# Kernel optimization log

Hardware: AMD Instinct MI355X
Metric: run time of the kernel (lower is better)

## Reference

```python
import jax, jax.numpy as jnp
import numpy as np

N = 50000   # nodes
E = 800000  # edges (avg degree 16)
D = 2048    # resnet50 feature dim
C = 256     # layer_size
NEG_SLOPE = 0.2


def setup_inputs() -> dict:
    key = jax.random.key(0)
    ks = jax.random.split(key, 16)
    s = 0.02
    inp = {
        'x': jax.random.normal(ks[0], (N, D), jnp.float32),
        'edge_index': jax.random.randint(ks[1], (2, E), 0, N, dtype=jnp.int32),
        # GATConv layer 1 (in=D, out=C, heads=1)
        'W1': jax.random.normal(ks[2], (D, C), jnp.float32) * s,
        'a_src1': jax.random.normal(ks[3], (C,), jnp.float32) * s,
        'a_dst1': jax.random.normal(ks[4], (C,), jnp.float32) * s,
        'b1': jnp.zeros((C,), jnp.float32),
        # GATConv layer 2 (in=C, out=C)
        'W2': jax.random.normal(ks[5], (C, C), jnp.float32) * s,
        'a_src2': jax.random.normal(ks[6], (C,), jnp.float32) * s,
        'a_dst2': jax.random.normal(ks[7], (C,), jnp.float32) * s,
        'b2': jnp.zeros((C,), jnp.float32),
        # EdgePredictor: lin1 (2C -> C), lin2 (C -> 1)
        'Wp1': jax.random.normal(ks[8], (2 * C, C), jnp.float32) * s,
        'bp1': jnp.zeros((C,), jnp.float32),
        'wp2': jax.random.normal(ks[9], (C,), jnp.float32) * s,
        'bp2': jnp.zeros((), jnp.float32),
    }
    return inp


def gat_layer(x, src, dst, W, a_src, a_dst, b, n_nodes):
    # PyG GATConv, heads=1, concat=True: message flows src -> dst,
    # softmax over incoming edges of each dst node.
    h = x @ W                                   # [N, C]
    e = jax.nn.leaky_relu((h @ a_src)[src] + (h @ a_dst)[dst], NEG_SLOPE)  # [E]
    emax = jax.ops.segment_max(e, dst, num_segments=n_nodes)
    ex = jnp.exp(e - emax[dst])
    denom = jax.ops.segment_sum(ex, dst, num_segments=n_nodes)
    alpha = ex / (denom[dst] + 1e-16)           # [E]
    out = jax.ops.segment_sum(h[src] * alpha[:, None], dst, num_segments=n_nodes)
    return out + b


def reference(x, edge_index, W1, a_src1, a_dst1, b1, W2, a_src2, a_dst2, b2,
              Wp1, bp1, wp2, bp2):
    src, dst = edge_index[0], edge_index[1]
    # GATConv default add_self_loops=True
    loops = jnp.arange(N, dtype=src.dtype)
    src_sl = jnp.concatenate([src, loops])
    dst_sl = jnp.concatenate([dst, loops])

    h = gat_layer(x, src_sl, dst_sl, W1, a_src1, a_dst1, b1, N)
    h = gat_layer(h, src_sl, dst_sl, W2, a_src2, a_dst2, b2, N)

    # edge predictor on the ORIGINAL edge_index (no self loops)
    xe = jnp.concatenate([h[src], h[dst]], axis=-1)       # [E, 2C]
    z = jax.nn.relu(xe @ Wp1 + bp1)                        # [E, C]  (dropout: eval mode)
    return z @ wp2 + bp2                                   # [E]
```

## Files before the change

kernel.cpp:

```cpp
#include <hip/hip_runtime.h>
#include <hip/hip_bf16.h>
#include <stdint.h>

#define NNODES 50000
#define NEDGES 800000
#define DIN    2048
#define CDIM   256
#define ELOOP  (NEDGES + NNODES)

using bf16x8 = __attribute__((ext_vector_type(8))) short;
using f32x4  = __attribute__((ext_vector_type(4))) float;
using gvoid  = __attribute__((address_space(1))) const void;
using lvoid  = __attribute__((address_space(3))) void;

__device__ __forceinline__ float bf2f(uint16_t u) {
    union { uint32_t i; float f; } v; v.i = (uint32_t)u << 16; return v.f;
}
__device__ __forceinline__ uint16_t f2bf(float f) {
    union { float f; uint32_t i; } v; v.f = f;
    uint32_t i = v.i;
    return (uint16_t)((i + 0x7FFFu + ((i >> 16) & 1u)) >> 16);
}
__device__ __forceinline__ void unpack8(uint4 r, float* f) {
    f[0] = bf2f((uint16_t)(r.x & 0xffffu)); f[1] = bf2f((uint16_t)(r.x >> 16));
    f[2] = bf2f((uint16_t)(r.y & 0xffffu)); f[3] = bf2f((uint16_t)(r.y >> 16));
    f[4] = bf2f((uint16_t)(r.z & 0xffffu)); f[5] = bf2f((uint16_t)(r.z >> 16));
    f[6] = bf2f((uint16_t)(r.w & 0xffffu)); f[7] = bf2f((uint16_t)(r.w >> 16));
}

#define BM 128
#define BN 128
#define BK 32

#define WAITVM(N) asm volatile("s_waitcnt vmcnt(" #N ")" ::: "memory")

#define ROWDOT_EPILOGUE()                                                     \
    if (s_src) {                                                              \
        float av[4], dv[4];                                                   \
        for (int nt2 = 0; nt2 < 4; ++nt2) {                                   \
            int gn = bn + wn + nt2 * 16 + lm;                                 \
            av[nt2] = asrc[gn];                                               \
            dv[nt2] = adst[gn];                                               \
        }                                                                     \
        for (int mt = 0; mt < 4; ++mt)                                        \
            for (int r = 0; r < 4; ++r) {                                     \
                float ps = 0.f, pd = 0.f;                                     \
                for (int nt2 = 0; nt2 < 4; ++nt2) {                           \
                    float v = acc[mt][nt2][r];                                \
                    ps += v * av[nt2];                                        \
                    pd += v * dv[nt2];                                        \
                }                                                             \
                for (int d = 1; d < 16; d <<= 1) {                            \
                    ps += __shfl_xor(ps, d);                                  \
                    pd += __shfl_xor(pd, d);                                  \
                }                                                             \
                if (lm == 0) {                                                \
                    int gm = bm + wm + mt * 16 + lq * 4 + r;                  \
                    if (gm < M) {                                             \
                        atomicAdd(&s_src[gm], ps);                            \
                        atomicAdd(&s_dst[gm], pd);                            \
                    }                                                         \
                }                                                             \
            }                                                                 \
    }

__global__ __launch_bounds__(256)
void gemm_bt(const uint16_t* __restrict__ A, const uint16_t* __restrict__ Bt,
             uint16_t* __restrict__ C, const float* __restrict__ bias,
             const float* __restrict__ asrc, const float* __restrict__ adst,
             float* __restrict__ s_src, float* __restrict__ s_dst,
             int M, int N, int K)
{
    __shared__ __align__(16) uint16_t lA[3][BM * BK];
    __shared__ __align__(16) uint16_t lB[3][BN * BK];
    const int tid  = threadIdx.x;
    const int wave = tid >> 6;
    const int lane = tid & 63;
    const int lm = lane & 15, lq = lane >> 4;
    const int bm = blockIdx.x * BM;
    const int bn = blockIdx.y * BN;
    const int wm = (wave >> 1) * 64;
    const int wn = (wave & 1) * 64;

    f32x4 acc[4][4];
    for (int i = 0; i < 4; ++i)
        for (int j = 0; j < 4; ++j)
            acc[i][j] = (f32x4)0.0f;

    auto stage = [&](int buf, int k0) {
        for (int j = 0; j < 2; ++j) {
            int c = j * 256 + wave * 64 + lane;
            int row = c >> 2, cc = c & 3;
            int gr = bm + row; if (gr >= M) gr = M - 1;
            const uint16_t* gp = A + (size_t)gr * K + k0 + cc * 8;
            __builtin_amdgcn_global_load_lds((gvoid*)gp,
                (lvoid*)(lA[buf] + (size_t)(j * 256 + wave * 64) * 8), 16, 0, 0);
        }
        for (int j = 0; j < 2; ++j) {
            int c = j * 256 + wave * 64 + lane;
            int row = c >> 2, cc = c & 3;
            const uint16_t* gp = Bt + (size_t)(bn + row) * K + k0 + cc * 8;
            __builtin_amdgcn_global_load_lds((gvoid*)gp,
                (lvoid*)(lB[buf] + (size_t)(j * 256 + wave * 64) * 8), 16, 0, 0);
        }
    };

    const int ntiles = K / BK;
    stage(0, 0);
    stage(1, BK);
    WAITVM(4);
    __builtin_amdgcn_s_barrier();

    for (int t = 0; t < ntiles; ++t) {
        const int cur = t % 3;
        if (t + 2 < ntiles) stage((t + 2) % 3, (t + 2) * BK);

        bf16x8 af[4], bfr[4];
        for (int mt = 0; mt < 4; ++mt)
            af[mt] = *(const bf16x8*)(lA[cur] + (wm + mt * 16 + lm) * BK + lq * 8);
        for (int nt2 = 0; nt2 < 4; ++nt2)
            bfr[nt2] = *(const bf16x8*)(lB[cur] + (wn + nt2 * 16 + lm) * BK + lq * 8);

        for (int mt = 0; mt < 4; ++mt)
            for (int nt2 = 0; nt2 < 4; ++nt2)
                acc[mt][nt2] = __builtin_amdgcn_mfma_f32_16x16x32_bf16(
                    af[mt], bfr[nt2], acc[mt][nt2], 0, 0, 0);

        if (t + 1 < ntiles) {
            if (t + 2 < ntiles) WAITVM(4);
            else                WAITVM(0);
            __builtin_amdgcn_s_barrier();
        }
    }

    for (int mt = 0; mt < 4; ++mt) {
        for (int nt2 = 0; nt2 < 4; ++nt2) {
            int gn = bn + wn + nt2 * 16 + lm;
            float badd = bias ? bias[gn] : 0.0f;
            for (int r = 0; r < 4; ++r) {
                int gm = bm + wm + mt * 16 + lq * 4 + r;
                if (gm < M)
                    C[(size_t)gm * N + gn] = f2bf(acc[mt][nt2][r] + badd);
            }
        }
    }

    ROWDOT_EPILOGUE();
}

__global__ __launch_bounds__(256)
void gemm_f32_bt(const float* __restrict__ A, const uint16_t* __restrict__ Bt,
                 uint16_t* __restrict__ C,
                 const float* __restrict__ asrc, const float* __restrict__ adst,
                 float* __restrict__ s_src, float* __restrict__ s_dst,
                 int M, int N, int K)
{
    __shared__ __align__(16) float    lA[3][BM * BK];
    __shared__ __align__(16) uint16_t lB[3][BN * BK];
    const int tid  = threadIdx.x;
    const int wave = tid >> 6;
    const int lane = tid & 63;
    const int lm = lane & 15, lq = lane >> 4;
    const int bm = blockIdx.x * BM;
    const int bn = blockIdx.y * BN;
    const int wm = (wave >> 1) * 64;
    const int wn = (wave & 1) * 64;

    f32x4 acc[4][4];
    for (int i = 0; i < 4; ++i)
        for (int j = 0; j < 4; ++j)
            acc[i][j] = (f32x4)0.0f;

    auto stage = [&](int buf, int k0) {
        for (int j = 0; j < 4; ++j) {
            int c = j * 256 + wave * 64 + lane;
            int row = c >> 3;
            int lc  = (c & 7) ^ (row & 7);
            int gr = bm + row; if (gr >= M) gr = M - 1;
            const float* gp = A + (size_t)gr * K + k0 + lc * 4;
            __builtin_amdgcn_global_load_lds((gvoid*)gp,
                (lvoid*)(lA[buf] + (size_t)(j * 256 + wave * 64) * 4), 16, 0, 0);
        }
        for (int j = 0; j < 2; ++j) {
            int c = j * 256 + wave * 64 + lane;
            int row = c >> 2, cc = c & 3;
            const uint16_t* gp = Bt + (size_t)(bn + row) * K + k0 + cc * 8;
            __builtin_amdgcn_global_load_lds((gvoid*)gp,
                (lvoid*)(lB[buf] + (size_t)(j * 256 + wave * 64) * 8), 16, 0, 0);
        }
    };

    const int ntiles = K / BK;
    stage(0, 0);
    stage(1, BK);
    WAITVM(6);
    __builtin_amdgcn_s_barrier();

    for (int t = 0; t < ntiles; ++t) {
        const int cur = t % 3;
        if (t + 2 < ntiles) stage((t + 2) % 3, (t + 2) * BK);

        bf16x8 af[4], bfr[4];
        for (int mt = 0; mt < 4; ++mt) {
            int r = wm + mt * 16 + lm;
            int s0 = (lq * 2)     ^ (r & 7);
            int s1 = (lq * 2 + 1) ^ (r & 7);
            f32x4 a0 = *(const f32x4*)(lA[cur] + r * BK + s0 * 4);
            f32x4 a1 = *(const f32x4*)(lA[cur] + r * BK + s1 * 4);
            union { uint32_t u[4]; bf16x8 v; } t2;
            float x0 = a0[0], x1 = a0[1], x2 = a0[2], x3 = a0[3];
            float y0 = a1[0], y1 = a1[1], y2 = a1[2], y3 = a1[3];
            asm("v_cvt_pk_bf16_f32 %0, %1, %2" : "=v"(t2.u[0]) : "v"(x0), "v"(x1));
            asm("v_cvt_pk_bf16_f32 %0, %1, %2" : "=v"(t2.u[1]) : "v"(x2), "v"(x3));
            asm("v_cvt_pk_bf16_f32 %0, %1, %2" : "=v"(t2.u[2]) : "v"(y0), "v"(y1));
            asm("v_cvt_pk_bf16_f32 %0, %1, %2" : "=v"(t2.u[3]) : "v"(y2), "v"(y3));
            af[mt] = t2.v;
        }
        for (int nt2 = 0; nt2 < 4; ++nt2)
            bfr[nt2] = *(const bf16x8*)(lB[cur] + (wn + nt2 * 16 + lm) * BK + lq * 8);

        for (int mt = 0; mt < 4; ++mt)
            for (int nt2 = 0; nt2 < 4; ++nt2)
                acc[mt][nt2] = __builtin_amdgcn_mfma_f32_16x16x32_bf16(
                    af[mt], bfr[nt2], acc[mt][nt2], 0, 0, 0);

        if (t + 1 < ntiles) {
            if (t + 2 < ntiles) WAITVM(6);
            else                WAITVM(0);
            __builtin_amdgcn_s_barrier();
        }
    }

    for (int mt = 0; mt < 4; ++mt) {
        for (int nt2 = 0; nt2 < 4; ++nt2) {
            int gn = bn + wn + nt2 * 16 + lm;
            for (int r = 0; r < 4; ++r) {
                int gm = bm + wm + mt * 16 + lq * 4 + r;
                if (gm < M)
                    C[(size_t)gm * N + gn] = f2bf(acc[mt][nt2][r]);
            }
        }
    }

    ROWDOT_EPILOGUE();
}

__global__ __launch_bounds__(256)
void transpose_cvt_kernel(const float* __restrict__ W,
                          uint16_t* __restrict__ Wt, int K, int N)
{
    __shared__ float tile[32][33];
    const int k0 = blockIdx.x * 32, n0 = blockIdx.y * 32;
    const int tx = threadIdx.x & 31, ty = threadIdx.x >> 5;
    for (int r = 0; r < 32; r += 8)
        tile[ty + r][tx] = W[(size_t)(k0 + ty + r) * N + n0 + tx];
    __syncthreads();
    for (int r = 0; r < 32; r += 8)
        Wt[(size_t)(n0 + ty + r) * K + k0 + tx] = f2bf(tile[tx][ty + r]);
}

__global__ void bias512_kernel(const float* __restrict__ bp1,
                               float* __restrict__ bias512)
{
    int i = blockIdx.x * 256 + threadIdx.x;
    if (i < 512) bias512[i] = (i < 256) ? bp1[i] : 0.0f;
}

__global__ void count_kernel(const int* __restrict__ ei, int* __restrict__ rs)
{
    int i = blockIdx.x * 256 + threadIdx.x;
    if (i >= ELOOP) return;
    int dst = (i < NEDGES) ? ei[NEDGES + i] : (i - NEDGES);
    atomicAdd(&rs[dst + 1], 1);
}

__global__ __launch_bounds__(1024)
void scan_part_kernel(int* __restrict__ rs, int* __restrict__ bsum)
{
    __shared__ int wsum[16];
    const int b = blockIdx.x, tid = threadIdx.x, lane = tid & 63, w = tid >> 6;
    int i = b * 1024 + tid;
    int v = (i <= NNODES) ? rs[i] : 0;
    int s = v;
    for (int d = 1; d < 64; d <<= 1) {
        int t = __shfl_up(s, d);
        if (lane >= d) s += t;
    }
    if (lane == 63) wsum[w] = s;
    __syncthreads();
    if (tid < 16) {
        int x = wsum[tid];
        for (int d = 1; d < 16; d <<= 1) {
            int t = __shfl_up(x, d);
            if (tid >= d) x += t;
        }
        wsum[tid] = x;
    }
    __syncthreads();
    int incl = s + (w > 0 ? wsum[w - 1] : 0);
    if (i <= NNODES) rs[i] = incl;
    if (tid == 1023) bsum[b] = incl;
}

__global__ void scan_bsum_kernel(int* __restrict__ bsum, int nb)
{
    int tid = threadIdx.x;
    int v = (tid < nb) ? bsum[tid] : 0;
    for (int d = 1; d < 64; d <<= 1) {
        int t = __shfl_up(v, d);
        if (tid >= d) v += t;
    }
    if (tid < nb) bsum[tid] = v;
}

__global__ __launch_bounds__(1024)
void scan_add_kernel(const int* __restrict__ bsum, int* __restrict__ rs,
                     int* __restrict__ cursor)
{
    int b = blockIdx.x;
    int i = b * 1024 + threadIdx.x;
    int add = b ? bsum[b - 1] : 0;
    if (i <= NNODES) {
        int r = rs[i] + add;
        rs[i] = r;
        if (i < NNODES) cursor[i] = r;
    }
}

__global__ void fill_kernel(const int* __restrict__ ei, int* __restrict__ cursor,
                            int* __restrict__ csr_src, int* __restrict__ csr_eid)
{
    int i = blockIdx.x * 256 + threadIdx.x;
    if (i >= ELOOP) return;
    int src, dst, eid;
    if (i < NEDGES) { src = ei[i]; dst = ei[NEDGES + i]; eid = i; }
    else            { src = dst = i - NEDGES; eid = -1; }
    int pos = atomicAdd(&cursor[dst], 1);
    csr_src[pos] = src;
    csr_eid[pos] = eid;
}

__global__ __launch_bounds__(256)
void attn_kernel(const int* __restrict__ row_start, const int* __restrict__ csr_src,
                 const float* __restrict__ s_src, const float* __restrict__ s_dst,
                 const uint16_t* __restrict__ g, const float* __restrict__ bvec,
                 uint16_t* __restrict__ hout)
{
    int n = blockIdx.x * 4 + (threadIdx.x >> 6);
    int lane = threadIdx.x & 63;
    int beg = row_start[n], end = row_start[n + 1];
    float sdn = s_dst[n];

    float m = -1e30f;
    for (int i = beg + lane; i < end; i += 64) {
        float e = s_src[csr_src[i]] + sdn;
        e = (e > 0.f) ? e : 0.2f * e;
        m = fmaxf(m, e);
    }
    for (int d = 32; d; d >>= 1) m = fmaxf(m, __shfl_xor(m, d));

    float sum = 0.f;
    for (int i = beg + lane; i < end; i += 64) {
        float e = s_src[csr_src[i]] + sdn;
        e = (e > 0.f) ? e : 0.2f * e;
        sum += __expf(e - m);
    }
    for (int d = 32; d; d >>= 1) sum += __shfl_xor(sum, d);
    float inv = 1.f / (sum + 1e-16f);

    const int q = lane >> 4, ql = lane & 15;
    float a[16];
    #pragma unroll
    for (int j = 0; j < 16; ++j) a[j] = 0.f;

    for (int i = beg + q; i < end; i += 4) {
        int src = csr_src[i];
        float e = s_src[src] + sdn;
        e = (e > 0.f) ? e : 0.2f * e;
        float alpha = __expf(e - m) * inv;
        const uint16_t* gp = g + (size_t)src * CDIM + ql * 16;
        uint4 r0 = *(const uint4*)gp;
        uint4 r1 = *(const uint4*)(gp + 8);
        float f0[8], f1[8];
        unpack8(r0, f0); unpack8(r1, f1);
        #pragma unroll
        for (int j = 0; j < 8; ++j) {
            a[j]     += alpha * f0[j];
            a[8 + j] += alpha * f1[j];
        }
    }
    #pragma unroll
    for (int j = 0; j < 16; ++j) {
        a[j] += __shfl_xor(a[j], 16);
        a[j] += __shfl_xor(a[j], 32);
    }

    if (q == 0) {
        const float4 b0 = *(const float4*)(bvec + ql * 16);
        const float4 b1 = *(const float4*)(bvec + ql * 16 + 4);
        const float4 b2 = *(const float4*)(bvec + ql * 16 + 8);
        const float4 b3 = *(const float4*)(bvec + ql * 16 + 12);
        uint4 o0, o1;
        o0.x = (uint32_t)f2bf(a[0]  + b0.x) | ((uint32_t)f2bf(a[1]  + b0.y) << 16);
        o0.y = (uint32_t)f2bf(a[2]  + b0.z) | ((uint32_t)f2bf(a[3]  + b0.w) << 16);
        o0.z = (uint32_t)f2bf(a[4]  + b1.x) | ((uint32_t)f2bf(a[5]  + b1.y) << 16);
        o0.w = (uint32_t)f2bf(a[6]  + b1.z) | ((uint32_t)f2bf(a[7]  + b1.w) << 16);
        o1.x = (uint32_t)f2bf(a[8]  + b2.x) | ((uint32_t)f2bf(a[9]  + b2.y) << 16);
        o1.y = (uint32_t)f2bf(a[10] + b2.z) | ((uint32_t)f2bf(a[11] + b2.w) << 16);
        o1.z = (uint32_t)f2bf(a[12] + b3.x) | ((uint32_t)f2bf(a[13] + b3.y) << 16);
        o1.w = (uint32_t)f2bf(a[14] + b3.z) | ((uint32_t)f2bf(a[15] + b3.w) << 16);
        uint16_t* op = hout + (size_t)n * CDIM + ql * 16;
        *(uint4*)op = o0;
        *(uint4*)(op + 8) = o1;
    }
}

__global__ __launch_bounds__(256)
void edgepred_kernel(const int* __restrict__ row_start,
                     const int* __restrict__ csr_src,
                     const int* __restrict__ csr_eid,
                     const uint16_t* __restrict__ UV,
                     const float* __restrict__ wp2, const float* __restrict__ bp2,
                     float* __restrict__ out)
{
    int n = blockIdx.x * 4 + (threadIdx.x >> 6);
    int lane = threadIdx.x & 63;
    int h = lane >> 5, hl = lane & 31;
    int beg = row_start[n], end = row_start[n + 1];

    uint4 vv = *(const uint4*)(UV + (size_t)n * 512 + 256 + hl * 8);
    float v[8];
    unpack8(vv, v);
    const float4 wa = *(const float4*)(wp2 + hl * 8);
    const float4 wb = *(const float4*)(wp2 + hl * 8 + 4);
    const float bp = *bp2;

    for (int i = beg + h; i < end; i += 2) {
        int eid = csr_eid[i];
        if (eid < 0) continue;
        int src = csr_src[i];
        uint4 uu = *(const uint4*)(UV + (size_t)src * 512 + hl * 8);
        float u[8];
        unpack8(uu, u);
        float acc;
        {
            float z0 = fmaxf(u[0] + v[0], 0.f), z1 = fmaxf(u[1] + v[1], 0.f);
            float z2 = fmaxf(u[2] + v[2], 0.f), z3 = fmaxf(u[3] + v[3], 0.f);
            float z4 = fmaxf(u[4] + v[4], 0.f), z5 = fmaxf(u[5] + v[5], 0.f);
            float z6 = fmaxf(u[6] + v[6], 0.f), z7 = fmaxf(u[7] + v[7], 0.f);
            acc = z0 * wa.x + z1 * wa.y + z2 * wa.z + z3 * wa.w
                + z4 * wb.x + z5 * wb.y + z6 * wb.z + z7 * wb.w;
        }
        for (int d = 1; d < 32; d <<= 1) acc += __shfl_xor(acc, d);
        if (hl == 0) out[eid] = acc + bp;
    }
}

extern "C" void kernel_launch(void* const* d_in, const int* in_sizes, int n_in,
                              void* d_out, int out_size, void* d_ws, size_t ws_size,
                              hipStream_t stream)
{
    const float* x   = (const float*)d_in[0];
    const int*   ei  = (const int*)d_in[1];
    const float* W1  = (const float*)d_in[2];
    const float* as1 = (const float*)d_in[3];
    const float* ad1 = (const float*)d_in[4];
    const float* b1  = (const float*)d_in[5];
    const float* W2  = (const float*)d_in[6];
    const float* as2 = (const float*)d_in[7];
    const float* ad2 = (const float*)d_in[8];
    const float* b2  = (const float*)d_in[9];
    const float* Wp1 = (const float*)d_in[10];
    const float* bp1 = (const float*)d_in[11];
    const float* wp2 = (const float*)d_in[12];
    const float* bp2 = (const float*)d_in[13];
    float* out = (float*)d_out;

    char* ws = (char*)d_ws;
    size_t off = 0;
    auto alloc = [&](size_t bytes) -> void* {
        void* p = ws + off;
        off += (bytes + 255) & ~(size_t)255;
        return p;
    };
    uint16_t* W1t   = (uint16_t*)alloc((size_t)DIN * CDIM * 2);
    uint16_t* W2t   = (uint16_t*)alloc((size_t)CDIM * CDIM * 2);
    uint16_t* WpABt = (uint16_t*)alloc((size_t)2 * CDIM * CDIM * 2);
    int* row_start = (int*)alloc((NNODES + 1) * sizeof(int));
    int* cursor    = (int*)alloc(NNODES * sizeof(int));
    int* csr_src   = (int*)alloc((size_t)ELOOP * sizeof(int));
    int* csr_eid   = (int*)alloc((size_t)ELOOP * sizeof(int));
    int* bsum      = (int*)alloc(64 * sizeof(int));
    float* sbuf    = (float*)alloc((size_t)2 * NNODES * sizeof(float));
    float* s_src   = sbuf;
    float* s_dst   = sbuf + NNODES;
    float* bias512 = (float*)alloc(512 * sizeof(float));
    uint16_t* H    = (uint16_t*)alloc((size_t)NNODES * CDIM * 2);
    uint16_t* G    = (uint16_t*)alloc((size_t)NNODES * CDIM * 2);
    uint16_t* Vb   = (uint16_t*)alloc((size_t)NNODES * CDIM * 2);
    (void)Vb;
    uint16_t* UV   = G;

    hipMemsetAsync(row_start, 0, (NNODES + 1) * sizeof(int), stream);
    hipMemsetAsync(sbuf, 0, (size_t)2 * NNODES * sizeof(float), stream);

    transpose_cvt_kernel<<<dim3(DIN / 32, CDIM / 32), 256, 0, stream>>>(W1, W1t, DIN, CDIM);
    transpose_cvt_kernel<<<dim3(CDIM / 32, CDIM / 32), 256, 0, stream>>>(W2, W2t, CDIM, CDIM);
    transpose_cvt_kernel<<<dim3(CDIM / 32, CDIM / 32), 256, 0, stream>>>(Wp1, WpABt, CDIM, CDIM);
    transpose_cvt_kernel<<<dim3(CDIM / 32, CDIM / 32), 256, 0, stream>>>(Wp1 + CDIM * CDIM, WpABt + CDIM * CDIM, CDIM, CDIM);
    bias512_kernel<<<2, 256, 0, stream>>>(bp1, bias512);

    const int NB = (NNODES + 1 + 1023) / 1024;
    count_kernel<<<(ELOOP + 255) / 256, 256, 0, stream>>>(ei, row_start);
    scan_part_kernel<<<NB, 1024, 0, stream>>>(row_start, bsum);
    scan_bsum_kernel<<<1, 64, 0, stream>>>(bsum, NB);
    scan_add_kernel<<<NB, 1024, 0, stream>>>(bsum, row_start, cursor);
    fill_kernel<<<(ELOOP + 255) / 256, 256, 0, stream>>>(ei, cursor, csr_src, csr_eid);

    dim3 gg((NNODES + BM - 1) / BM, CDIM / BN);

    gemm_f32_bt<<<gg, 256, 0, stream>>>(x, W1t, G, as1, ad1, s_src, s_dst,
                                        NNODES, CDIM, DIN);
    attn_kernel<<<NNODES / 4, 256, 0, stream>>>(row_start, csr_src, s_src, s_dst, G, b1, H);

    hipMemsetAsync(sbuf, 0, (size_t)2 * NNODES * sizeof(float), stream);
    gemm_bt<<<gg, 256, 0, stream>>>(H, W2t, G, nullptr, as2, ad2, s_src, s_dst,
                                    NNODES, CDIM, CDIM);
    attn_kernel<<<NNODES / 4, 256, 0, stream>>>(row_start, csr_src, s_src, s_dst, G, b2, H);

    dim3 gg2((NNODES + BM - 1) / BM, 512 / BN);
    gemm_bt<<<gg2, 256, 0, stream>>>(H, WpABt, UV, bias512, nullptr, nullptr,
                                     nullptr, nullptr, NNODES, 512, CDIM);

    edgepred_kernel<<<NNODES / 4, 256, 0, stream>>>(row_start, csr_src, csr_eid,
                                                    UV, wp2, bp2, out);
}
```

Measured before the change: 1.086 ms.

## Cache attention logits in LDS, widen gathers, merge weight transposes

The attention kernel now caches each node's neighbor indices and leaky-relu logits in shared memory (up to 96 per node). This avoids recomputing the s_src gathers in the sum and aggregation passes, and the aggregation processes 8 edges per wave with 32 channels per lane. The edge predictor processes 4 edges per wave with 16 channels per lane, and the four weight transpose launches are merged into one 3D-grid launch. The changes raise register pressure in attn_kernel (32 accumulators) and make the 256-channel reduction cost more shuffles.

```diff
diff --git a/kernel.cpp b/kernel.cpp
--- a/kernel.cpp
+++ b/kernel.cpp
@@ -7,6 +7,7 @@
 #define DIN    2048
 #define CDIM   256
 #define ELOOP  (NEDGES + NNODES)
+#define DCAP   96
 
 using bf16x8 = __attribute__((ext_vector_type(8))) short;
 using f32x4  = __attribute__((ext_vector_type(4))) float;
@@ -246,11 +247,22 @@
 }
 
 __global__ __launch_bounds__(256)
-void transpose_cvt_kernel(const float* __restrict__ W,
-                          uint16_t* __restrict__ Wt, int K, int N)
+void transpose_cvt4_kernel(const float* __restrict__ W1,
+                           const float* __restrict__ W2,
+                           const float* __restrict__ Wp1,
+                           uint16_t* __restrict__ W1t,
+                           uint16_t* __restrict__ W2t,
+                           uint16_t* __restrict__ WpABt)
 {
     __shared__ float tile[32][33];
+    const int z = blockIdx.z;
+    const float* W; uint16_t* Wt; int K, N;
+    if (z == 0)      { W = W1;                Wt = W1t;                K = DIN;  N = CDIM; }
+    else if (z == 1) { W = W2;                Wt = W2t;                K = CDIM; N = CDIM; }
+    else if (z == 2) { W = Wp1;               Wt = WpABt;              K = CDIM; N = CDIM; }
+    else             { W = Wp1 + CDIM * CDIM; Wt = WpABt + CDIM * CDIM; K = CDIM; N = CDIM; }
     const int k0 = blockIdx.x * 32, n0 = blockIdx.y * 32;
+    if (k0 >= K) return;
     const int tx = threadIdx.x & 31, ty = threadIdx.x >> 5;
     for (int r = 0; r < 32; r += 8)
         tile[ty + r][tx] = W[(size_t)(k0 + ty + r) * N + n0 + tx];
@@ -346,72 +358,89 @@
                  const uint16_t* __restrict__ g, const float* __restrict__ bvec,
                  uint16_t* __restrict__ hout)
 {
-    int n = blockIdx.x * 4 + (threadIdx.x >> 6);
+    __shared__ int   lsrc[4][DCAP];
+    __shared__ float le[4][DCAP];
+    const int w = threadIdx.x >> 6;
+    int n = blockIdx.x * 4 + w;
     int lane = threadIdx.x & 63;
     int beg = row_start[n], end = row_start[n + 1];
+    int deg = end - beg;
     float sdn = s_dst[n];
 
     float m = -1e30f;
-    for (int i = beg + lane; i < end; i += 64) {
-        float e = s_src[csr_src[i]] + sdn;
+    for (int idx = lane; idx < deg; idx += 64) {
+        int src = csr_src[beg + idx];
+        float e = s_src[src] + sdn;
         e = (e > 0.f) ? e : 0.2f * e;
+        if (idx < DCAP) { lsrc[w][idx] = src; le[w][idx] = e; }
         m = fmaxf(m, e);
     }
     for (int d = 32; d; d >>= 1) m = fmaxf(m, __shfl_xor(m, d));
+    asm volatile("s_waitcnt lgkmcnt(0)" ::: "memory");
 
     float sum = 0.f;
-    for (int i = beg + lane; i < end; i += 64) {
-        float e = s_src[csr_src[i]] + sdn;
-        e = (e > 0.f) ? e : 0.2f * e;
+    for (int idx = lane; idx < deg; idx += 64) {
+        float e;
+        if (idx < DCAP) e = le[w][idx];
+        else {
+            int src = csr_src[beg + idx];
+            e = s_src[src] + sdn;
+            e = (e > 0.f) ? e : 0.2f * e;
+        }
         sum += __expf(e - m);
     }
     for (int d = 32; d; d >>= 1) sum += __shfl_xor(sum, d);
     float inv = 1.f / (sum + 1e-16f);
 
-    const int q = lane >> 4, ql = lane & 15;
-    float a[16];
+    const int gq = lane >> 3, gl = lane & 7;
+    float a[32];
     #pragma unroll
-    for (int j = 0; j < 16; ++j) a[j] = 0.f;
-
-    for (int i = beg + q; i < end; i += 4) {
-        int src = csr_src[i];
-        float e = s_src[src] + sdn;
-        e = (e > 0.f) ? e : 0.2f * e;
+    for (int j = 0; j < 32; ++j) a[j] = 0.f;
+
+    for (int idx = gq; idx < deg; idx += 8) {
+        int src; float e;
+        if (idx < DCAP) { src = lsrc[w][idx]; e = le[w][idx]; }
+        else {
+            src = csr_src[beg + idx];
+            e = s_src[src] + sdn;
+            e = (e > 0.f) ? e : 0.2f * e;
+        }
         float alpha = __expf(e - m) * inv;
-        const uint16_t* gp = g + (size_t)src * CDIM + ql * 16;
+        const uint16_t* gp = g + (size_t)src * CDIM + gl * 32;
         uint4 r0 = *(const uint4*)gp;
         uint4 r1 = *(const uint4*)(gp + 8);
-        float f0[8], f1[8];
-        unpack8(r0, f0); unpack8(r1, f1);
+        uint4 r2 = *(const uint4*)(gp + 16);
+        uint4 r3 = *(const uint4*)(gp + 24);
+        float f0[8], f1[8], f2[8], f3[8];
+        unpack8(r0, f0); unpack8(r1, f1); unpack8(r2, f2); unpack8(r3, f3);
         #pragma unroll
         for (int j = 0; j < 8; ++j) {
-            a[j]     += alpha * f0[j];
-            a[8 + j] += alpha * f1[j];
+            a[j]      += alpha * f0[j];
+            a[8 + j]  += alpha * f1[j];
+            a[16 + j] += alpha * f2[j];
+            a[24 + j] += alpha * f3[j];
         }
     }
     #pragma unroll
-    for (int j = 0; j < 16; ++j) {
+    for (int j = 0; j < 32; ++j) {
+        a[j] += __shfl_xor(a[j], 8);
         a[j] += __shfl_xor(a[j], 16);
         a[j] += __shfl_xor(a[j], 32);
     }
 
-    if (q == 0) {
-        const float4 b0 = *(const float4*)(bvec + ql * 16);
-        const float4 b1 = *(const float4*)(bvec + ql * 16 + 4);
-        const float4 b2 = *(const float4*)(bvec + ql * 16 + 8);
-        const float4 b3 = *(const float4*)(bvec + ql * 16 + 12);
-        uint4 o0, o1;
-        o0.x = (uint32_t)f2bf(a[0]  + b0.x) | ((uint32_t)f2bf(a[1]  + b0.y) << 16);
-        o0.y = (uint32_t)f2bf(a[2]  + b0.z) | ((uint32_t)f2bf(a[3]  + b0.w) << 16);
-        o0.z = (uint32_t)f2bf(a[4]  + b1.x) | ((uint32_t)f2bf(a[5]  + b1.y) << 16);
-        o0.w = (uint32_t)f2bf(a[6]  + b1.z) | ((uint32_t)f2bf(a[7]  + b1.w) << 16);
-        o1.x = (uint32_t)f2bf(a[8]  + b2.x) | ((uint32_t)f2bf(a[9]  + b2.y) << 16);
-        o1.y = (uint32_t)f2bf(a[10] + b2.z) | ((uint32_t)f2bf(a[11] + b2.w) << 16);
-        o1.z = (uint32_t)f2bf(a[12] + b3.x) | ((uint32_t)f2bf(a[13] + b3.y) << 16);
-        o1.w = (uint32_t)f2bf(a[14] + b3.z) | ((uint32_t)f2bf(a[15] + b3.w) << 16);
-        uint16_t* op = hout + (size_t)n * CDIM + ql * 16;
-        *(uint4*)op = o0;
-        *(uint4*)(op + 8) = o1;
+    if (gq == 0) {
+        uint16_t* op = hout + (size_t)n * CDIM + gl * 32;
+        #pragma unroll
+        for (int blk = 0; blk < 4; ++blk) {
+            const float4 ba = *(const float4*)(bvec + gl * 32 + blk * 8);
+            const float4 bb = *(const float4*)(bvec + gl * 32 + blk * 8 + 4);
+            uint4 o;
+            o.x = (uint32_t)f2bf(a[blk*8+0] + ba.x) | ((uint32_t)f2bf(a[blk*8+1] + ba.y) << 16);
+            o.y = (uint32_t)f2bf(a[blk*8+2] + ba.z) | ((uint32_t)f2bf(a[blk*8+3] + ba.w) << 16);
+            o.z = (uint32_t)f2bf(a[blk*8+4] + bb.x) | ((uint32_t)f2bf(a[blk*8+5] + bb.y) << 16);
+            o.w = (uint32_t)f2bf(a[blk*8+6] + bb.z) | ((uint32_t)f2bf(a[blk*8+7] + bb.w) << 16);
+            *(uint4*)(op + blk * 8) = o;
+        }
     }
 }
 
@@ -425,34 +454,37 @@
 {
     int n = blockIdx.x * 4 + (threadIdx.x >> 6);
     int lane = threadIdx.x & 63;
-    int h = lane >> 5, hl = lane & 31;
+    int q = lane >> 4, ql = lane & 15;
     int beg = row_start[n], end = row_start[n + 1];
 
-    uint4 vv = *(const uint4*)(UV + (size_t)n * 512 + 256 + hl * 8);
-    float v[8];
-    unpack8(vv, v);
-    const float4 wa = *(const float4*)(wp2 + hl * 8);
-    const float4 wb = *(const float4*)(wp2 + hl * 8 + 4);
+    const uint16_t* vp = UV + (size_t)n * 512 + 256 + ql * 16;
+    uint4 v0 = *(const uint4*)vp;
+    uint4 v1 = *(const uint4*)(vp + 8);
+    float v[16];
+    unpack8(v0, v); unpack8(v1, v + 8);
+    float wv[16];
+    #pragma unroll
+    for (int j = 0; j < 16; j += 4) {
+        float4 wq = *(const float4*)(wp2 + ql * 16 + j);
+        wv[j] = wq.x; wv[j+1] = wq.y; wv[j+2] = wq.z; wv[j+3] = wq.w;
+    }
     const float bp = *bp2;
 
-    for (int i = beg + h; i < end; i += 2) {
+    for (int i = beg + q; i < end; i += 4) {
         int eid = csr_eid[i];
         if (eid < 0) continue;
         int src = csr_src[i];
-        uint4 uu = *(const uint4*)(UV + (size_t)src * 512 + hl * 8);
-        float u[8];
-        unpack8(uu, u);
-        float acc;
-        {
-            float z0 = fmaxf(u[0] + v[0], 0.f), z1 = fmaxf(u[1] + v[1], 0.f);
-            float z2 = fmaxf(u[2] + v[2], 0.f), z3 = fmaxf(u[3] + v[3], 0.f);
-            float z4 = fmaxf(u[4] + v[4], 0.f), z5 = fmaxf(u[5] + v[5], 0.f);
-            float z6 = fmaxf(u[6] + v[6], 0.f), z7 = fmaxf(u[7] + v[7], 0.f);
-            acc = z0 * wa.x + z1 * wa.y + z2 * wa.z + z3 * wa.w
-                + z4 * wb.x + z5 * wb.y + z6 * wb.z + z7 * wb.w;
-        }
-        for (int d = 1; d < 32; d <<= 1) acc += __shfl_xor(acc, d);
-        if (hl == 0) out[eid] = acc + bp;
+        const uint16_t* up = UV + (size_t)src * 512 + ql * 16;
+        uint4 u0 = *(const uint4*)up;
+        uint4 u1 = *(const uint4*)(up + 8);
+        float u[16];
+        unpack8(u0, u); unpack8(u1, u + 8);
+        float acc = 0.f;
+        #pragma unroll
+        for (int j = 0; j < 16; ++j)
+            acc += fmaxf(u[j] + v[j], 0.f) * wv[j];
+        for (int d = 1; d < 16; d <<= 1) acc += __shfl_xor(acc, d);
+        if (ql == 0) out[eid] = acc + bp;
     }
 }
 
@@ -504,10 +536,8 @@
     hipMemsetAsync(row_start, 0, (NNODES + 1) * sizeof(int), stream);
     hipMemsetAsync(sbuf, 0, (size_t)2 * NNODES * sizeof(float), stream);
 
-    transpose_cvt_kernel<<<dim3(DIN / 32, CDIM / 32), 256, 0, stream>>>(W1, W1t, DIN, CDIM);
-    transpose_cvt_kernel<<<dim3(CDIM / 32, CDIM / 32), 256, 0, stream>>>(W2, W2t, CDIM, CDIM);
-    transpose_cvt_kernel<<<dim3(CDIM / 32, CDIM / 32), 256, 0, stream>>>(Wp1, WpABt, CDIM, CDIM);
-    transpose_cvt_kernel<<<dim3(CDIM / 32, CDIM / 32), 256, 0, stream>>>(Wp1 + CDIM * CDIM, WpABt + CDIM * CDIM, CDIM, CDIM);
+    transpose_cvt4_kernel<<<dim3(DIN / 32, CDIM / 32, 4), 256, 0, stream>>>(
+        W1, W2, Wp1, W1t, W2t, WpABt);
     bias512_kernel<<<2, 256, 0, stream>>>(bp1, bias512);
 
     const int NB = (NNODES + 1 + 1023) / 1024;
```

Measured after the change: 1.082 ms. Within noise of the previous version (-0.3%).
